# Kernel tuning notes

Hardware: AMD Instinct MI355X
Metric: run time of the kernel (lower is better)

## Reference

```python
import jax, jax.numpy as jnp
import numpy as np

B, H, W, C = 2, 128, 128, 256
WS = 8            # current_window (query window)
KW = 16           # halo_window = 2*current_window
HEADS = 8
HD = C // HEADS
PRETRAIN = 8
CPB_HIDDEN = 512


def _rel_bias_consts():
    halo = (KW - WS) // 2
    coords = np.arange(1 - WS - halo, WS + halo, dtype=np.float32)  # length WS+KW-1 = 23
    tab = np.stack(np.meshgrid(coords, coords, indexing='ij'), axis=-1)  # [23,23,2]
    tab = tab * (8.0 / (PRETRAIN - 1.0))
    tab = np.sign(tab) * np.log1p(np.abs(tab)) / np.log(8.0)
    tab = tab.reshape(-1, 2).astype(np.float32)                      # [529,2]
    qi = np.arange(WS)
    qg = np.stack(np.meshgrid(qi, qi, indexing='ij')).reshape(2, -1)  # [2,64]
    ki = np.arange(KW)
    kg = np.stack(np.meshgrid(ki, ki, indexing='ij')).reshape(2, -1)  # [2,256]
    rel = qg[:, :, None] - kg[:, None] + (KW - 1)
    idx = (rel[0] * (WS + KW - 1) + rel[1]).reshape(-1).astype(np.int32)  # [64*256]
    return tab, idx

_REL_TAB, _REL_IDX = _rel_bias_consts()


def setup_inputs() -> dict:
    key = jax.random.key(0)
    ks = jax.random.split(key, 12)
    s = 0.02
    return {
        'x': jax.random.normal(ks[0], (B, H, W, C), jnp.float32),
        'w_qkv': jax.random.normal(ks[1], (C, 3 * C), jnp.float32) * s,
        'w_dw': jax.random.normal(ks[2], (3, 3, 1, 3 * C), jnp.float32) * s,  # depthwise HWIO
        'ln_g': jnp.ones((3 * C,), jnp.float32),
        'ln_b': jnp.zeros((3 * C,), jnp.float32),
        'q_bias': jnp.zeros((C,), jnp.float32),
        'v_bias': jnp.zeros((C,), jnp.float32),
        'logit_scale': jnp.full((HEADS, 1, 1), np.log(10.0), jnp.float32),
        'cpb_w1': jax.random.normal(ks[3], (2, CPB_HIDDEN), jnp.float32) * s,
        'cpb_b1': jnp.zeros((CPB_HIDDEN,), jnp.float32),
        'cpb_w2': jax.random.normal(ks[4], (CPB_HIDDEN, HEADS), jnp.float32) * s,
        'w_proj': jax.random.normal(ks[5], (C, C), jnp.float32) * s,
    }


def _l2n(t):
    # tf.math.l2_normalize with epsilon=1.55e-5
    return t * jax.lax.rsqrt(jnp.maximum(jnp.sum(t * t, -1, keepdims=True), 1.55e-5))


def reference(x, w_qkv, w_dw, ln_g, ln_b, q_bias, v_bias, logit_scale,
              cpb_w1, cpb_b1, cpb_w2, w_proj):
    nWh, nWw = H // WS, W // WS
    nW = nWh * nWw
    # qkv 1x1 conv + depthwise 3x3 + layernorm + (q,0,v) bias
    qkv = jnp.einsum('bhwc,cd->bhwd', x, w_qkv)
    qkv = jax.lax.conv_general_dilated(
        qkv, w_dw, (1, 1), 'SAME',
        dimension_numbers=('NHWC', 'HWIO', 'NHWC'), feature_group_count=3 * C)
    mu = jnp.mean(qkv, -1, keepdims=True)
    var = jnp.var(qkv, -1, keepdims=True)
    qkv = (qkv - mu) * jax.lax.rsqrt(var + 1e-5) * ln_g + ln_b
    qkv = qkv + jnp.concatenate([q_bias, jnp.zeros_like(q_bias), v_bias])
    q, kv = qkv[..., :C], qkv[..., C:]
    # window partition of q: [B*nW, heads, WS*WS, HD]
    qp = q.reshape(B, nWh, WS, nWw, WS, HEADS, HD)
    qp = qp.transpose(0, 1, 3, 5, 2, 4, 6).reshape(B * nW, HEADS, WS * WS, HD)
    # halo partition of kv: overlapping KWxKW patches, stride WS
    halo = (KW - WS) // 2
    kvp = jnp.pad(kv, ((0, 0), (halo, halo), (halo, halo), (0, 0)))
    ridx = (np.arange(nWh) * WS)[:, None] + np.arange(KW)[None]  # [nWh,KW]
    cidx = (np.arange(nWw) * WS)[:, None] + np.arange(KW)[None]  # [nWw,KW]
    kvp = kvp[:, ridx][:, :, :, cidx]               # [B,nWh,KW,nWw,KW,2C]
    kvp = kvp.transpose(0, 1, 3, 2, 4, 5).reshape(B * nW, KW * KW, 2, HEADS, HD)
    k = kvp[:, :, 0].transpose(0, 2, 1, 3)          # [B*nW, heads, KW*KW, HD]
    v = kvp[:, :, 1].transpose(0, 2, 1, 3)
    # cosine attention with clamped learned log-scale
    scale = jnp.exp(jnp.minimum(logit_scale, np.float32(np.log(100.0))))
    attn = jnp.einsum('whqd,whkd->whqk', _l2n(qp) * scale, _l2n(k))
    # continuous relative position bias (CPB MLP + gather)
    hidden = jax.nn.relu(jnp.asarray(_REL_TAB) @ cpb_w1 + cpb_b1)
    bias_tab = jax.nn.sigmoid(hidden @ cpb_w2) * 16.0        # [529, heads]
    rb = bias_tab[_REL_IDX].reshape(WS * WS, KW * KW, HEADS).transpose(2, 0, 1)
    attn = jax.nn.softmax(attn + rb[None], axis=-1)
    out = jnp.einsum('whqk,whkd->whqd', attn, v)             # [B*nW, heads, 64, HD]
    # reverse window partition
    out = out.reshape(B, nWh, nWw, HEADS, WS, WS, HD)
    out = out.transpose(0, 1, 4, 2, 5, 3, 6).reshape(B, H, W, C)
    return jnp.einsum('bhwc,cd->bhwd', out, w_proj)
```

## Files before the change

kernel.cpp:

```cpp
#include <hip/hip_runtime.h>
#include <hip/hip_bf16.h>
#include <hip/hip_fp16.h>
#include <cstddef>
#include <cstdint>

#define BB 2
#define HH 128
#define WW 128
#define CC 256
#define WSZ 8
#define KWIN 16
#define NHEADS 8
#define HD 32
#define C3 768
#define NPIX 32768
#define NWIN 512

typedef short    bf16x8 __attribute__((ext_vector_type(8)));
typedef _Float16 half8  __attribute__((ext_vector_type(8)));
typedef float    f32x4  __attribute__((ext_vector_type(4)));

#define LOG2E 1.4426950408889634f

#if __has_builtin(__builtin_amdgcn_exp2f)
#define EXP2(x) __builtin_amdgcn_exp2f(x)
#else
#define EXP2(x) __expf((x) * 0.6931471805599453f)
#endif

__device__ inline void gload_lds16(const _Float16* g, _Float16* l) {
    __builtin_amdgcn_global_load_lds(
        (const __attribute__((address_space(1))) unsigned int*)g,
        (__attribute__((address_space(3))) unsigned int*)l, 16, 0, 0);
}

__global__ __launch_bounds__(64) void cpb_kernel(const float* __restrict__ w1,
                                                 const float* __restrict__ b1,
                                                 const float* __restrict__ w2,
                                                 float* __restrict__ btab) {
    const int e = blockIdx.x;
    const int i = e / 23, j = e % 23;
    const float inv_log8 = 1.0f / logf(8.0f);
    float c0 = (float)(i - 11) * (8.0f / 7.0f);
    float c1 = (float)(j - 11) * (8.0f / 7.0f);
    float f0 = copysignf(log1pf(fabsf(c0)) * inv_log8, c0);
    float f1 = copysignf(log1pf(fabsf(c1)) * inv_log8, c1);

    const int t = threadIdx.x;
    float acc[8] = {0.f,0.f,0.f,0.f,0.f,0.f,0.f,0.f};
    for (int kk = 0; kk < 8; kk++) {
        int k = kk * 64 + t;
        float hid = f0 * w1[k] + f1 * w1[512 + k] + b1[k];
        hid = fmaxf(hid, 0.f);
        #pragma unroll
        for (int h = 0; h < 8; h++) acc[h] += hid * w2[k * 8 + h];
    }
    #pragma unroll
    for (int h = 0; h < 8; h++) {
        #pragma unroll
        for (int off = 32; off >= 1; off >>= 1) acc[h] += __shfl_xor(acc[h], off);
    }
    if (t < 8) {
        float v = acc[t];
        btab[e * 8 + t] = 16.0f / (1.0f + expf(-v));
    }
}

__global__ __launch_bounds__(256) void cvt_wdw(const float* __restrict__ src,
                                               _Float16* __restrict__ dst) {
    int i = blockIdx.x * 256 + threadIdx.x;
    if (i < 9 * C3) dst[i] = (_Float16)src[i];
}

__global__ __launch_bounds__(256) void transpose_cvt(const float* __restrict__ src,
                                                     _Float16* __restrict__ dst,
                                                     int R, int Cn) {
    __shared__ float t[32][33];
    const int bx = blockIdx.x, by = blockIdx.y;
    const int tx = threadIdx.x & 31, ty = threadIdx.x >> 5;
    #pragma unroll
    for (int i = 0; i < 4; i++) {
        int r = by * 32 + ty + i * 8;
        t[ty + i * 8][tx] = src[(size_t)r * Cn + bx * 32 + tx];
    }
    __syncthreads();
    #pragma unroll
    for (int i = 0; i < 4; i++) {
        int dr = bx * 32 + ty + i * 8;
        dst[(size_t)dr * R + by * 32 + tx] = (_Float16)t[tx][ty + i * 8];
    }
}

template <typename OT>
__global__ __launch_bounds__(256) void gemm_f16(const _Float16* __restrict__ A,
                                                const _Float16* __restrict__ Bt,
                                                OT* __restrict__ C,
                                                int M, int N, int K) {
    __shared__ _Float16 Ash[128][64];
    __shared__ _Float16 Bsh[128][64];
    const int tid = threadIdx.x;
    const int wv = tid >> 6, ln = tid & 63;
    const int quad = ln >> 4, l15 = ln & 15;
    const int rowb = blockIdx.y * 128;
    const int colb = blockIdx.x * 128;
    const int wm = (wv >> 1) * 64, wn = (wv & 1) * 64;

    const int r8 = ln >> 3, g = ln & 7;
    const int kg = g ^ r8;

    f32x4 acc[4][4] = {};
    for (int k0 = 0; k0 < K; k0 += 64) {
        #pragma unroll
        for (int i = 0; i < 4; i++) {
            const int m = wv * 32 + i * 8 + r8;
            gload_lds16(A + (size_t)(rowb + m) * K + k0 + kg * 8,
                        &Ash[wv * 32 + i * 8][0]);
            gload_lds16(Bt + (size_t)(colb + m) * K + k0 + kg * 8,
                        &Bsh[wv * 32 + i * 8][0]);
        }
        __syncthreads();
        #pragma unroll
        for (int kk = 0; kk < 2; kk++) {
            const int phys = ((kk * 4 + quad) ^ (l15 & 7)) * 8;
            half8 a[4], b[4];
            #pragma unroll
            for (int i = 0; i < 4; i++)
                a[i] = *(const half8*)&Ash[wm + i * 16 + l15][phys];
            #pragma unroll
            for (int j = 0; j < 4; j++)
                b[j] = *(const half8*)&Bsh[wn + j * 16 + l15][phys];
            #pragma unroll
            for (int i = 0; i < 4; i++)
                #pragma unroll
                for (int j = 0; j < 4; j++)
                    acc[i][j] = __builtin_amdgcn_mfma_f32_16x16x32_f16(
                        a[i], b[j], acc[i][j], 0, 0, 0);
        }
        __syncthreads();
    }
    #pragma unroll
    for (int i = 0; i < 4; i++) {
        #pragma unroll
        for (int reg = 0; reg < 4; reg++) {
            const size_t row = rowb + wm + i * 16 + quad * 4 + reg;
            #pragma unroll
            for (int j = 0; j < 4; j++) {
                C[row * N + colb + wn + j * 16 + l15] = (OT)acc[i][j][reg];
            }
        }
    }
}

__global__ __launch_bounds__(256) void gemm_qkv(const float* __restrict__ A,
                                                const _Float16* __restrict__ Bt,
                                                _Float16* __restrict__ C,
                                                int M, int N, int K) {
    __shared__ _Float16 Ash[128][64];
    __shared__ _Float16 Bsh[128][64];
    const int tid = threadIdx.x;
    const int wv = tid >> 6, ln = tid & 63;
    const int quad = ln >> 4, l15 = ln & 15;
    const int rowb = blockIdx.y * 128;
    const int colb = blockIdx.x * 128;
    const int wm = (wv >> 1) * 64, wn = (wv & 1) * 64;
    const int r8 = ln >> 3, g = ln & 7;
    const int kg = g ^ r8;

    f32x4 acc[4][4] = {};
    for (int k0 = 0; k0 < K; k0 += 64) {
        #pragma unroll
        for (int i = 0; i < 4; i++) {
            const int m = wv * 32 + i * 8 + r8;
            const float* ap = A + (size_t)(rowb + m) * K + k0 + g * 8;
            const float4 a0 = *(const float4*)ap;
            const float4 a1 = *(const float4*)(ap + 4);
            half8 hv;
            hv[0] = (_Float16)a0.x; hv[1] = (_Float16)a0.y;
            hv[2] = (_Float16)a0.z; hv[3] = (_Float16)a0.w;
            hv[4] = (_Float16)a1.x; hv[5] = (_Float16)a1.y;
            hv[6] = (_Float16)a1.z; hv[7] = (_Float16)a1.w;
            *(half8*)&Ash[wv * 32 + i * 8 + r8][kg * 8] = hv;
            gload_lds16(Bt + (size_t)(colb + m) * K + k0 + kg * 8,
                        &Bsh[wv * 32 + i * 8][0]);
        }
        __syncthreads();
        #pragma unroll
        for (int kk = 0; kk < 2; kk++) {
            const int phys = ((kk * 4 + quad) ^ (l15 & 7)) * 8;
            half8 a[4], b[4];
            #pragma unroll
            for (int i = 0; i < 4; i++)
                a[i] = *(const half8*)&Ash[wm + i * 16 + l15][phys];
            #pragma unroll
            for (int j = 0; j < 4; j++)
                b[j] = *(const half8*)&Bsh[wn + j * 16 + l15][phys];
            #pragma unroll
            for (int i = 0; i < 4; i++)
                #pragma unroll
                for (int j = 0; j < 4; j++)
                    acc[i][j] = __builtin_amdgcn_mfma_f32_16x16x32_f16(
                        a[i], b[j], acc[i][j], 0, 0, 0);
        }
        __syncthreads();
    }
    #pragma unroll
    for (int i = 0; i < 4; i++) {
        #pragma unroll
        for (int reg = 0; reg < 4; reg++) {
            const size_t row = rowb + wm + i * 16 + quad * 4 + reg;
            #pragma unroll
            for (int j = 0; j < 4; j++) {
                C[row * N + colb + wn + j * 16 + l15] = (_Float16)acc[i][j][reg];
            }
        }
    }
}

__global__ __launch_bounds__(256) void dwconv_ln(const _Float16* __restrict__ in,
                                                 const _Float16* __restrict__ wdwh,
                                                 const float* __restrict__ g,
                                                 const float* __restrict__ bt,
                                                 const float* __restrict__ qb,
                                                 const float* __restrict__ vb,
                                                 const float* __restrict__ logit_scale,
                                                 _Float16* __restrict__ out) {
    __shared__ __align__(16) _Float16 S[2][960 * 8];
    __shared__ float sred[4][8][2];

    const int t = threadIdx.x;
    const int pix0 = blockIdx.x * 8;
    const int b = pix0 >> 14, y = (pix0 >> 7) & 127, x0 = pix0 & 127;
    const int p = t & 7, gidx = t >> 3;

    const float lsc_q = __expf(fminf(logit_scale[gidx >> 2], 4.60517019f)) * LOG2E;

    const _Float16* sp[4];
    int sphys[4];
    bool sok[4];
    #pragma unroll
    for (int k = 0; k < 4; k++) {
        const int u = t + k * 256;
        const int cell = u >> 5, grp = u & 31;
        const int r = (cell >= 20) ? 2 : (cell >= 10 ? 1 : 0);
        const int c = cell - r * 10;
        const int yy = y + r - 1, xx = x0 + c - 1;
        const bool inb = ((unsigned)yy < 128u) && ((unsigned)xx < 128u);
        sok[k] = inb;
        sp[k] = in + (((size_t)(b * 128 + (inb ? yy : 0)) * 128 + (inb ? xx : 0)) * C3)
                   + grp * 8;
        sphys[k] = (u & ~7) | ((u ^ c) & 7);
    }

    auto STAGE = [&](int s, int buf) {
        #pragma unroll
        for (int k = 0; k < 4; k++) {
            if (k < 3 || t < 192) {
                half8 v = (half8)(_Float16)0;
                if (sok[k]) v = *(const half8*)(sp[k] + s * 256);
                *(half8*)&S[buf][sphys[k] * 8] = v;
            }
        }
    };

    STAGE(0, 0);
    float acc[3][8] = {};
    #pragma unroll
    for (int s = 0; s < 3; s++) {
        __syncthreads();
        if (s < 2) STAGE(s + 1, (s + 1) & 1);
        const _Float16* Sb = &S[s & 1][0];
        half8 w[9];
        #pragma unroll
        for (int tap = 0; tap < 9; tap++)
            w[tap] = *(const half8*)(wdwh + (tap * 96 + s * 32 + gidx) * 8);
        #pragma unroll
        for (int r = 0; r < 3; r++) {
            #pragma unroll
            for (int dx = 0; dx < 3; dx++) {
                const int cc = p + dx;
                const int u = (r * 10 + cc) * 32 + gidx;
                const int phys = (u & ~7) | ((u ^ cc) & 7);
                const half8 v = *(const half8*)&Sb[phys * 8];
                const half8 wt = w[r * 3 + dx];
                #pragma unroll
                for (int i = 0; i < 8; i++)
                    acc[s][i] += (float)v[i] * (float)wt[i];
            }
        }
    }

    float ls = 0.f, lss = 0.f;
    #pragma unroll
    for (int s = 0; s < 3; s++)
        #pragma unroll
        for (int i = 0; i < 8; i++) { ls += acc[s][i]; lss += acc[s][i] * acc[s][i]; }
    ls  += __shfl_xor(ls, 8);  lss += __shfl_xor(lss, 8);
    ls  += __shfl_xor(ls, 16); lss += __shfl_xor(lss, 16);
    ls  += __shfl_xor(ls, 32); lss += __shfl_xor(lss, 32);
    const int wv = t >> 6, lnid = t & 63;
    if (lnid < 8) { sred[wv][lnid][0] = ls; sred[wv][lnid][1] = lss; }
    __syncthreads();
    const float Ssum  = sred[0][p][0] + sred[1][p][0] + sred[2][p][0] + sred[3][p][0];
    const float SSsum = sred[0][p][1] + sred[1][p][1] + sred[2][p][1] + sred[3][p][1];
    const float mu  = Ssum * (1.0f / 768.0f);
    const float var = SSsum * (1.0f / 768.0f) - mu * mu;
    const float rs  = rsqrtf(var + 1e-5f);

    const size_t obase = (size_t)(pix0 + p) * C3;
    #pragma unroll
    for (int s = 0; s < 3; s++) {
        const int ch = gidx * 8 + s * 256;
        const float4 g0 = *(const float4*)(g + ch);
        const float4 g1 = *(const float4*)(g + ch + 4);
        const float4 b0 = *(const float4*)(bt + ch);
        const float4 b1 = *(const float4*)(bt + ch + 4);
        float gg[8] = {g0.x, g0.y, g0.z, g0.w, g1.x, g1.y, g1.z, g1.w};
        float bb[8] = {b0.x, b0.y, b0.z, b0.w, b1.x, b1.y, b1.z, b1.w};
        if (s == 0) {
            const float4 e0 = *(const float4*)(qb + ch);
            const float4 e1 = *(const float4*)(qb + ch + 4);
            bb[0] += e0.x; bb[1] += e0.y; bb[2] += e0.z; bb[3] += e0.w;
            bb[4] += e1.x; bb[5] += e1.y; bb[6] += e1.z; bb[7] += e1.w;
        } else if (s == 2) {
            const float4 e0 = *(const float4*)(vb + ch - 512);
            const float4 e1 = *(const float4*)(vb + ch - 512 + 4);
            bb[0] += e0.x; bb[1] += e0.y; bb[2] += e0.z; bb[3] += e0.w;
            bb[4] += e1.x; bb[5] += e1.y; bb[6] += e1.z; bb[7] += e1.w;
        }
        float of[8];
        #pragma unroll
        for (int i = 0; i < 8; i++)
            of[i] = (acc[s][i] - mu) * rs * gg[i] + bb[i];
        if (s < 2) {
            float s2 = 0.f;
            #pragma unroll
            for (int i = 0; i < 8; i++) s2 += of[i] * of[i];
            s2 += __shfl_xor(s2, 8);
            s2 += __shfl_xor(s2, 16);
            float scl = rsqrtf(fmaxf(s2, 1.55e-5f));
            if (s == 0) scl *= lsc_q;
            #pragma unroll
            for (int i = 0; i < 8; i++) of[i] *= scl;
        }
        half8 o;
        #pragma unroll
        for (int i = 0; i < 8; i++) o[i] = (_Float16)of[i];
        *(half8*)(out + obase + ch) = o;
    }
}

#define P2SHIFT 14.0f

__global__ __launch_bounds__(256) void attn_mfma(const _Float16* __restrict__ qkv,
                                                 const float* __restrict__ bias_tab,
                                                 const float* __restrict__ logit_scale,
                                                 _Float16* __restrict__ out) {
    const int blk = blockIdx.x;
    const int h = blk & 7;
    const int wid = blk >> 3;
    const int b = wid >> 8;
    const int wy = (wid >> 4) & 15;
    const int wx = wid & 15;
    const int tid = threadIdx.x;
    const int wave = tid >> 6, lane = tid & 63;
    const int quad = lane >> 4, l15 = lane & 15;

    __shared__ __align__(16) _Float16 Bf[16 * 64 * 8];
    __shared__ __align__(16) _Float16 Vt2[1024 * 8];
    __shared__ float btab[529];

    const float lscale = __expf(fminf(logit_scale[h], 4.60517019f));
    const float MshiftL2 = (lscale + 16.0f) * LOG2E - P2SHIFT;
    for (int e = tid; e < 529; e += 256)
        btab[e] = bias_tab[e * 8 + h] * LOG2E - MshiftL2;

    {
        const int j = tid;
        const int kr = j >> 4, kcc = j & 15;
        const int gy = wy * 8 - 4 + kr, gx = wx * 8 - 4 + kcc;
        const bool inb = ((unsigned)gy < 128u) && ((unsigned)gx < 128u);
        const _Float16* p = qkv +
            (((size_t)(b * 128 + (inb ? gy : 0)) * 128 + (inb ? gx : 0)) * C3) +
            256 + h * HD;
        const int nt  = ((j >> 5) << 1) | ((j >> 2) & 1);
        const int pos = (((j >> 3) & 3) << 2) | (j & 3);
        const int ch_ = j >> 5, qq = (j >> 3) & 3, uu = j & 7;
        const int swz = ((qq & 1) << 2) | ((ch_ & 1) << 1);
        #pragma unroll
        for (int d8 = 0; d8 < 4; d8++) {
            half8 kk, vv;
            if (inb) { kk = *(const half8*)(p + d8 * 8); vv = *(const half8*)(p + 256 + d8 * 8); }
            else     { kk = (half8)(_Float16)0;          vv = (half8)(_Float16)0; }
            *(half8*)&Bf[((nt * 64) + d8 * 16 + pos) * 8] = kk;
            #pragma unroll
            for (int u2 = 0; u2 < 8; u2++) {
                const int d = d8 * 8 + u2;
                const int unit = ((ch_ * 2 + (d >> 4)) * 64) + qq * 16 + ((d & 15) ^ swz);
                Vt2[unit * 8 + uu] = vv[u2];
            }
        }
    }

    const int qrow = wave * 16 + l15;
    const int qr = qrow >> 3, qc = qrow & 7;
    const int qy = wy * 8 + qr, qx = wx * 8 + qc;
    const half8 qfrag = *(const half8*)(qkv +
        (((size_t)(b * 128 + qy) * 128 + qx) * C3) + h * HD + quad * 8);
    __syncthreads();

    const int colbase = qc + 15 - ((quad & 1) << 3);
    const int rowq    = qr + 15 - (quad >> 1);
    const int rsw     = (quad & 1) << 2;
    float lsum = 0.f;
    f32x4 d0 = {0.f, 0.f, 0.f, 0.f};
    f32x4 d1 = {0.f, 0.f, 0.f, 0.f};
    #pragma unroll
    for (int ch = 0; ch < 8; ch++) {
        const half8 ka0 = *(const half8*)&Bf[((2 * ch)     * 64 + lane) * 8];
        const half8 ka1 = *(const half8*)&Bf[((2 * ch + 1) * 64 + lane) * 8];
        const float* bt = &btab[(rowq - 2 * ch) * 23 + colbase];
        f32x4 s0 = {bt[0],  bt[-1], bt[-2], bt[-3]};
        f32x4 s1 = {bt[-4], bt[-5], bt[-6], bt[-7]};
        __builtin_amdgcn_s_setprio(1);
        s0 = __builtin_amdgcn_mfma_f32_16x16x32_f16(ka0, qfrag, s0, 0, 0, 0);
        s1 = __builtin_amdgcn_mfma_f32_16x16x32_f16(ka1, qfrag, s1, 0, 0, 0);
        __builtin_amdgcn_s_setprio(0);
        half8 pa;
        #pragma unroll
        for (int r = 0; r < 4; r++) {
            const float p0 = EXP2(s0[r]);
            const float p1 = EXP2(s1[r]);
            lsum += p0 + p1;
            pa[r]     = (_Float16)p0;
            pa[4 + r] = (_Float16)p1;
        }
        const int lsw = l15 ^ (rsw | ((ch & 1) << 1));
        const half8 v0 = *(const half8*)&Vt2[(((ch * 2 + 0) * 64) + quad * 16 + lsw) * 8];
        const half8 v1 = *(const half8*)&Vt2[(((ch * 2 + 1) * 64) + quad * 16 + lsw) * 8];
        __builtin_amdgcn_s_setprio(1);
        d0 = __builtin_amdgcn_mfma_f32_16x16x32_f16(pa, v0, d0, 0, 0, 0);
        d1 = __builtin_amdgcn_mfma_f32_16x16x32_f16(pa, v1, d1, 0, 0, 0);
        __builtin_amdgcn_s_setprio(0);
    }

    lsum += __shfl_xor(lsum, 16);
    lsum += __shfl_xor(lsum, 32);
    const float inv = 1.0f / lsum;

    #pragma unroll
    for (int reg = 0; reg < 4; reg++) {
        const int q = quad * 4 + reg;
        const float invq = __shfl(inv, q);
        const int gq = wave * 16 + q;
        const int oqr = gq >> 3, oqc = gq & 7;
        const int oy = wy * 8 + oqr, ox = wx * 8 + oqc;
        _Float16* op = out + (((size_t)(b * 128 + oy) * 128 + ox) * CC) + h * HD;
        op[l15]      = (_Float16)(d0[reg] * invq);
        op[16 + l15] = (_Float16)(d1[reg] * invq);
    }
}

extern "C" void kernel_launch(void* const* d_in, const int* in_sizes, int n_in,
                              void* d_out, int out_size, void* d_ws, size_t ws_size,
                              hipStream_t stream) {
    const float* x           = (const float*)d_in[0];
    const float* w_qkv       = (const float*)d_in[1];
    const float* w_dw        = (const float*)d_in[2];
    const float* ln_g        = (const float*)d_in[3];
    const float* ln_b        = (const float*)d_in[4];
    const float* q_bias      = (const float*)d_in[5];
    const float* v_bias      = (const float*)d_in[6];
    const float* logit_scale = (const float*)d_in[7];
    const float* cpb_w1      = (const float*)d_in[8];
    const float* cpb_b1      = (const float*)d_in[9];
    const float* cpb_w2      = (const float*)d_in[10];
    const float* w_proj      = (const float*)d_in[11];
    float* out = (float*)d_out;

    char* ws = (char*)d_ws;
    _Float16* attnh  = (_Float16*)(ws);
    _Float16* qkvh   = (_Float16*)(ws + 16777216);
    _Float16* qkv0h  = (_Float16*)(ws + 67108864);
    _Float16* wqkvT  = (_Float16*)(ws + 117440512);
    _Float16* wprojT = (_Float16*)(ws + 117833728);
    _Float16* wdwh   = (_Float16*)(ws + 117964800);
    float*    btab   = (float*)   (ws + 117981184);

    cpb_kernel<<<529, 64, 0, stream>>>(cpb_w1, cpb_b1, cpb_w2, btab);
    cvt_wdw<<<27, 256, 0, stream>>>(w_dw, wdwh);
    transpose_cvt<<<dim3(C3 / 32, CC / 32), 256, 0, stream>>>(w_qkv, wqkvT, CC, C3);
    transpose_cvt<<<dim3(CC / 32, CC / 32), 256, 0, stream>>>(w_proj, wprojT, CC, CC);

    gemm_qkv<<<dim3(C3 / 128, NPIX / 128), 256, 0, stream>>>(
        x, wqkvT, qkv0h, NPIX, C3, CC);
    dwconv_ln<<<NPIX / 8, 256, 0, stream>>>(qkv0h, wdwh, ln_g, ln_b, q_bias,
                                            v_bias, logit_scale, qkvh);
    attn_mfma<<<NWIN * NHEADS, 256, 0, stream>>>(qkvh, btab, logit_scale, attnh);
    gemm_f16<float><<<dim3(CC / 128, NPIX / 128), 256, 0, stream>>>(
        attnh, wprojT, out, NPIX, CC, CC);
}
```

Before: 240.3 us.

## Tile dwconv over 2x8 pixels and simplify attention V layout to padded transpose

The depthwise-conv+LayerNorm kernel now processes a 2-row by 8-pixel tile per block instead of one 8-pixel row. The 4x10 halo is staged once for both rows, which cuts redundant halo loads roughly from 3x to 2x per output row, and each thread handles two channel groups. The attention kernel replaces the swizzled Vt2 layout with a simple padded transpose Vt[32][264], which simplifies indexing but may change LDS bank conflicts on both the scatter writes and the vector reads. The block count for dwconv is halved, reducing parallelism and raising per-thread register use.

```diff
diff --git a/kernel.cpp b/kernel.cpp
--- a/kernel.cpp
+++ b/kernel.cpp
@@ -224,67 +224,77 @@
                                                  const float* __restrict__ vb,
                                                  const float* __restrict__ logit_scale,
                                                  _Float16* __restrict__ out) {
-    __shared__ __align__(16) _Float16 S[2][960 * 8];
-    __shared__ float sred[4][8][2];
+    __shared__ __align__(16) _Float16 S[2][1280 * 8];
+    float* sred = (float*)&S[0][0];
 
     const int t = threadIdx.x;
-    const int pix0 = blockIdx.x * 8;
-    const int b = pix0 >> 14, y = (pix0 >> 7) & 127, x0 = pix0 & 127;
-    const int p = t & 7, gidx = t >> 3;
-
-    const float lsc_q = __expf(fminf(logit_scale[gidx >> 2], 4.60517019f)) * LOG2E;
-
-    const _Float16* sp[4];
-    int sphys[4];
-    bool sok[4];
-    #pragma unroll
-    for (int k = 0; k < 4; k++) {
+    const int bid = blockIdx.x;
+    const int b   = bid >> 10;
+    const int rem = bid & 1023;
+    const int ty  = rem >> 4;
+    const int tx  = rem & 15;
+    const int y0  = ty * 2, x0 = tx * 8;
+
+    const int w = t >> 6, l = t & 63;
+    const int py = w & 1, px = l & 7;
+    const int p  = py * 8 + px;
+    const int gs = (l >> 3) + ((w >> 1) << 3);
+
+    const float lsc0 = __expf(fminf(logit_scale[gs >> 2], 4.60517019f)) * LOG2E;
+    const float lsc1 = __expf(fminf(logit_scale[(gs >> 2) + 4], 4.60517019f)) * LOG2E;
+
+    const _Float16* sp[5];
+    int sphys[5];
+    bool sok[5];
+    #pragma unroll
+    for (int k = 0; k < 5; k++) {
         const int u = t + k * 256;
         const int cell = u >> 5, grp = u & 31;
-        const int r = (cell >= 20) ? 2 : (cell >= 10 ? 1 : 0);
-        const int c = cell - r * 10;
-        const int yy = y + r - 1, xx = x0 + c - 1;
+        const int rr = cell / 10, cc = cell - rr * 10;
+        const int yy = y0 + rr - 1, xx = x0 + cc - 1;
         const bool inb = ((unsigned)yy < 128u) && ((unsigned)xx < 128u);
         sok[k] = inb;
         sp[k] = in + (((size_t)(b * 128 + (inb ? yy : 0)) * 128 + (inb ? xx : 0)) * C3)
                    + grp * 8;
-        sphys[k] = (u & ~7) | ((u ^ c) & 7);
+        sphys[k] = (u & ~7) | ((u ^ cc) & 7);
     }
 
     auto STAGE = [&](int s, int buf) {
         #pragma unroll
-        for (int k = 0; k < 4; k++) {
-            if (k < 3 || t < 192) {
-                half8 v = (half8)(_Float16)0;
-                if (sok[k]) v = *(const half8*)(sp[k] + s * 256);
-                *(half8*)&S[buf][sphys[k] * 8] = v;
-            }
+        for (int k = 0; k < 5; k++) {
+            half8 v = (half8)(_Float16)0;
+            if (sok[k]) v = *(const half8*)(sp[k] + s * 256);
+            *(half8*)&S[buf][sphys[k] * 8] = v;
         }
     };
 
     STAGE(0, 0);
-    float acc[3][8] = {};
+    float acc[3][2][8] = {};
     #pragma unroll
     for (int s = 0; s < 3; s++) {
         __syncthreads();
         if (s < 2) STAGE(s + 1, (s + 1) & 1);
         const _Float16* Sb = &S[s & 1][0];
-        half8 w[9];
-        #pragma unroll
-        for (int tap = 0; tap < 9; tap++)
-            w[tap] = *(const half8*)(wdwh + (tap * 96 + s * 32 + gidx) * 8);
-        #pragma unroll
-        for (int r = 0; r < 3; r++) {
-            #pragma unroll
-            for (int dx = 0; dx < 3; dx++) {
-                const int cc = p + dx;
-                const int u = (r * 10 + cc) * 32 + gidx;
-                const int phys = (u & ~7) | ((u ^ cc) & 7);
-                const half8 v = *(const half8*)&Sb[phys * 8];
-                const half8 wt = w[r * 3 + dx];
+        #pragma unroll
+        for (int m = 0; m < 2; m++) {
+            const int grp = gs + m * 16;
+            half8 wv[9];
+            #pragma unroll
+            for (int tap = 0; tap < 9; tap++)
+                wv[tap] = *(const half8*)(wdwh + (tap * 96 + s * 32 + grp) * 8);
+            #pragma unroll
+            for (int dy = 0; dy < 3; dy++) {
                 #pragma unroll
-                for (int i = 0; i < 8; i++)
-                    acc[s][i] += (float)v[i] * (float)wt[i];
+                for (int dx = 0; dx < 3; dx++) {
+                    const int cc = px + dx;
+                    const int u = ((py + dy) * 10 + cc) * 32 + grp;
+                    const int phys = (u & ~7) | ((u ^ cc) & 7);
+                    const half8 v = *(const half8*)&Sb[phys * 8];
+                    const half8 wt = wv[dy * 3 + dx];
+                    #pragma unroll
+                    for (int i = 0; i < 8; i++)
+                        acc[s][m][i] += (float)v[i] * (float)wt[i];
+                }
             }
         }
     }
@@ -293,59 +303,67 @@
     #pragma unroll
     for (int s = 0; s < 3; s++)
         #pragma unroll
-        for (int i = 0; i < 8; i++) { ls += acc[s][i]; lss += acc[s][i] * acc[s][i]; }
+        for (int m = 0; m < 2; m++)
+            #pragma unroll
+            for (int i = 0; i < 8; i++) { ls += acc[s][m][i]; lss += acc[s][m][i] * acc[s][m][i]; }
     ls  += __shfl_xor(ls, 8);  lss += __shfl_xor(lss, 8);
     ls  += __shfl_xor(ls, 16); lss += __shfl_xor(lss, 16);
     ls  += __shfl_xor(ls, 32); lss += __shfl_xor(lss, 32);
-    const int wv = t >> 6, lnid = t & 63;
-    if (lnid < 8) { sred[wv][lnid][0] = ls; sred[wv][lnid][1] = lss; }
     __syncthreads();
-    const float Ssum  = sred[0][p][0] + sred[1][p][0] + sred[2][p][0] + sred[3][p][0];
-    const float SSsum = sred[0][p][1] + sred[1][p][1] + sred[2][p][1] + sred[3][p][1];
+    if (l < 8) {
+        sred[(((w >> 1) << 4) + (py << 3) + l) * 2 + 0] = ls;
+        sred[(((w >> 1) << 4) + (py << 3) + l) * 2 + 1] = lss;
+    }
+    __syncthreads();
+    const float Ssum  = sred[p * 2 + 0] + sred[(16 + p) * 2 + 0];
+    const float SSsum = sred[p * 2 + 1] + sred[(16 + p) * 2 + 1];
     const float mu  = Ssum * (1.0f / 768.0f);
     const float var = SSsum * (1.0f / 768.0f) - mu * mu;
     const float rs  = rsqrtf(var + 1e-5f);
 
-    const size_t obase = (size_t)(pix0 + p) * C3;
+    const size_t obase = (size_t)((b * 128 + y0 + py) * 128 + x0 + px) * C3;
     #pragma unroll
     for (int s = 0; s < 3; s++) {
-        const int ch = gidx * 8 + s * 256;
-        const float4 g0 = *(const float4*)(g + ch);
-        const float4 g1 = *(const float4*)(g + ch + 4);
-        const float4 b0 = *(const float4*)(bt + ch);
-        const float4 b1 = *(const float4*)(bt + ch + 4);
-        float gg[8] = {g0.x, g0.y, g0.z, g0.w, g1.x, g1.y, g1.z, g1.w};
-        float bb[8] = {b0.x, b0.y, b0.z, b0.w, b1.x, b1.y, b1.z, b1.w};
-        if (s == 0) {
-            const float4 e0 = *(const float4*)(qb + ch);
-            const float4 e1 = *(const float4*)(qb + ch + 4);
-            bb[0] += e0.x; bb[1] += e0.y; bb[2] += e0.z; bb[3] += e0.w;
-            bb[4] += e1.x; bb[5] += e1.y; bb[6] += e1.z; bb[7] += e1.w;
-        } else if (s == 2) {
-            const float4 e0 = *(const float4*)(vb + ch - 512);
-            const float4 e1 = *(const float4*)(vb + ch - 512 + 4);
-            bb[0] += e0.x; bb[1] += e0.y; bb[2] += e0.z; bb[3] += e0.w;
-            bb[4] += e1.x; bb[5] += e1.y; bb[6] += e1.z; bb[7] += e1.w;
-        }
-        float of[8];
-        #pragma unroll
-        for (int i = 0; i < 8; i++)
-            of[i] = (acc[s][i] - mu) * rs * gg[i] + bb[i];
-        if (s < 2) {
-            float s2 = 0.f;
-            #pragma unroll
-            for (int i = 0; i < 8; i++) s2 += of[i] * of[i];
-            s2 += __shfl_xor(s2, 8);
-            s2 += __shfl_xor(s2, 16);
-            float scl = rsqrtf(fmaxf(s2, 1.55e-5f));
-            if (s == 0) scl *= lsc_q;
-            #pragma unroll
-            for (int i = 0; i < 8; i++) of[i] *= scl;
-        }
-        half8 o;
-        #pragma unroll
-        for (int i = 0; i < 8; i++) o[i] = (_Float16)of[i];
-        *(half8*)(out + obase + ch) = o;
+        #pragma unroll
+        for (int m = 0; m < 2; m++) {
+            const int ch = (gs + m * 16) * 8 + s * 256;
+            const float4 g0 = *(const float4*)(g + ch);
+            const float4 g1 = *(const float4*)(g + ch + 4);
+            const float4 b0 = *(const float4*)(bt + ch);
+            const float4 b1 = *(const float4*)(bt + ch + 4);
+            float gg[8] = {g0.x, g0.y, g0.z, g0.w, g1.x, g1.y, g1.z, g1.w};
+            float bb[8] = {b0.x, b0.y, b0.z, b0.w, b1.x, b1.y, b1.z, b1.w};
+            if (s == 0) {
+                const float4 e0 = *(const float4*)(qb + ch);
+                const float4 e1 = *(const float4*)(qb + ch + 4);
+                bb[0] += e0.x; bb[1] += e0.y; bb[2] += e0.z; bb[3] += e0.w;
+                bb[4] += e1.x; bb[5] += e1.y; bb[6] += e1.z; bb[7] += e1.w;
+            } else if (s == 2) {
+                const float4 e0 = *(const float4*)(vb + ch - 512);
+                const float4 e1 = *(const float4*)(vb + ch - 512 + 4);
+                bb[0] += e0.x; bb[1] += e0.y; bb[2] += e0.z; bb[3] += e0.w;
+                bb[4] += e1.x; bb[5] += e1.y; bb[6] += e1.z; bb[7] += e1.w;
+            }
+            float of[8];
+            #pragma unroll
+            for (int i = 0; i < 8; i++)
+                of[i] = (acc[s][m][i] - mu) * rs * gg[i] + bb[i];
+            if (s < 2) {
+                float s2 = 0.f;
+                #pragma unroll
+                for (int i = 0; i < 8; i++) s2 += of[i] * of[i];
+                s2 += __shfl_xor(s2, 8);
+                s2 += __shfl_xor(s2, 16);
+                float scl = rsqrtf(fmaxf(s2, 1.55e-5f));
+                if (s == 0) scl *= (m ? lsc1 : lsc0);
+                #pragma unroll
+                for (int i = 0; i < 8; i++) of[i] *= scl;
+            }
+            half8 o;
+            #pragma unroll
+            for (int i = 0; i < 8; i++) o[i] = (_Float16)of[i];
+            *(half8*)(out + obase + ch) = o;
+        }
     }
 }
 
@@ -366,7 +384,7 @@
     const int quad = lane >> 4, l15 = lane & 15;
 
     __shared__ __align__(16) _Float16 Bf[16 * 64 * 8];
-    __shared__ __align__(16) _Float16 Vt2[1024 * 8];
+    __shared__ __align__(16) _Float16 Vt[32][264];
     __shared__ float btab[529];
 
     const float lscale = __expf(fminf(logit_scale[h], 4.60517019f));
@@ -384,8 +402,6 @@
             256 + h * HD;
         const int nt  = ((j >> 5) << 1) | ((j >> 2) & 1);
         const int pos = (((j >> 3) & 3) << 2) | (j & 3);
-        const int ch_ = j >> 5, qq = (j >> 3) & 3, uu = j & 7;
-        const int swz = ((qq & 1) << 2) | ((ch_ & 1) << 1);
         #pragma unroll
         for (int d8 = 0; d8 < 4; d8++) {
             half8 kk, vv;
@@ -393,11 +409,8 @@
             else     { kk = (half8)(_Float16)0;          vv = (half8)(_Float16)0; }
             *(half8*)&Bf[((nt * 64) + d8 * 16 + pos) * 8] = kk;
             #pragma unroll
-            for (int u2 = 0; u2 < 8; u2++) {
-                const int d = d8 * 8 + u2;
-                const int unit = ((ch_ * 2 + (d >> 4)) * 64) + qq * 16 + ((d & 15) ^ swz);
-                Vt2[unit * 8 + uu] = vv[u2];
-            }
+            for (int u = 0; u < 8; u++)
+                Vt[d8 * 8 + u][j] = vv[u];
         }
     }
 
@@ -410,7 +423,6 @@
 
     const int colbase = qc + 15 - ((quad & 1) << 3);
     const int rowq    = qr + 15 - (quad >> 1);
-    const int rsw     = (quad & 1) << 2;
     float lsum = 0.f;
     f32x4 d0 = {0.f, 0.f, 0.f, 0.f};
     f32x4 d1 = {0.f, 0.f, 0.f, 0.f};
@@ -434,9 +446,8 @@
             pa[r]     = (_Float16)p0;
             pa[4 + r] = (_Float16)p1;
         }
-        const int lsw = l15 ^ (rsw | ((ch & 1) << 1));
-        const half8 v0 = *(const half8*)&Vt2[(((ch * 2 + 0) * 64) + quad * 16 + lsw) * 8];
-        const half8 v1 = *(const half8*)&Vt2[(((ch * 2 + 1) * 64) + quad * 16 + lsw) * 8];
+        const half8 v0 = *(const half8*)&Vt[l15][ch * 32 + quad * 8];
+        const half8 v1 = *(const half8*)&Vt[l15 + 16][ch * 32 + quad * 8];
         __builtin_amdgcn_s_setprio(1);
         d0 = __builtin_amdgcn_mfma_f32_16x16x32_f16(pa, v0, d0, 0, 0, 0);
         d1 = __builtin_amdgcn_mfma_f32_16x16x32_f16(pa, v1, d1, 0, 0, 0);
@@ -493,8 +504,8 @@
 
     gemm_qkv<<<dim3(C3 / 128, NPIX / 128), 256, 0, stream>>>(
         x, wqkvT, qkv0h, NPIX, C3, CC);
-    dwconv_ln<<<NPIX / 8, 256, 0, stream>>>(qkv0h, wdwh, ln_g, ln_b, q_bias,
-                                            v_bias, logit_scale, qkvh);
+    dwconv_ln<<<NPIX / 16, 256, 0, stream>>>(qkv0h, wdwh, ln_g, ln_b, q_bias,
+                                             v_bias, logit_scale, qkvh);
     attn_mfma<<<NWIN * NHEADS, 256, 0, stream>>>(qkvh, btab, logit_scale, attnh);
     gemm_f16<float><<<dim3(CC / 128, NPIX / 128), 256, 0, stream>>>(
         attnh, wprojT, out, NPIX, CC, CC);
```

After: 246.0 us. 1.02x slower.
